# Optimization experiments

Measured on AMD Instinct MI355X. Metric: run time of the kernel, lower is better.

## Reference

```python
import jax, jax.numpy as jnp
import numpy as np

VOCAB, EMB = 32000, 300
B, T, S = 64, 25, 50
NF = 100
FS = (3, 4, 5)
H = 256
OUT = 31


def setup_inputs() -> dict:
    key = jax.random.key(0)
    ks = jax.random.split(key, 12)
    inp = {}
    inp["dialogue"] = jax.random.randint(ks[0], (B, T, S), 0, VOCAB)
    inp["emb"] = jax.random.normal(ks[1], (VOCAB, EMB), jnp.float32) * 0.1
    for j, fs in enumerate(FS):
        inp[f"conv_w{fs}"] = jax.random.normal(ks[2 + j], (NF, 1, fs, EMB), jnp.float32) * (1.0 / np.sqrt(fs * EMB))
        inp[f"conv_b{fs}"] = jnp.zeros((NF,), jnp.float32)
    IN = NF * len(FS)
    sc = 1.0 / np.sqrt(H)
    inp["wih"] = jax.random.normal(ks[5], (4 * H, IN), jnp.float32) * sc
    inp["whh"] = jax.random.normal(ks[6], (4 * H, H), jnp.float32) * sc
    inp["bih"] = jnp.zeros((4 * H,), jnp.float32)
    inp["bhh"] = jnp.zeros((4 * H,), jnp.float32)
    inp["wih_r"] = jax.random.normal(ks[7], (4 * H, IN), jnp.float32) * sc
    inp["whh_r"] = jax.random.normal(ks[8], (4 * H, H), jnp.float32) * sc
    inp["bih_r"] = jnp.zeros((4 * H,), jnp.float32)
    inp["bhh_r"] = jnp.zeros((4 * H,), jnp.float32)
    inp["h2o_w"] = jax.random.normal(ks[9], (OUT, 2 * H), jnp.float32) * sc
    inp["h2o_b"] = jnp.zeros((OUT,), jnp.float32)
    return inp


def _cnn_embed(tokens, emb, conv_params):
    # tokens: [B,T,S] int -> per-utterance CNN features [B,T, NF*len(FS)]
    x = emb[tokens.reshape(-1, S)]           # [B*T, S, EMB] embedding lookup
    x = x[:, None, :, :]                      # NCHW: [B*T, 1, S, EMB]
    feats = []
    for (w, b) in conv_params:
        c = jax.lax.conv_general_dilated(
            x, w, (1, 1), 'VALID', dimension_numbers=('NCHW', 'OIHW', 'NCHW'))
        c = jax.nn.relu(c + b[None, :, None, None])   # [B*T, NF, S-fs+1, 1]
        feats.append(jnp.max(c[..., 0], axis=2))      # max-pool over time -> [B*T, NF]
    return jnp.concatenate(feats, axis=1).reshape(B, T, -1)


def _lstm(x, wih, whh, bih, bhh):
    # single-layer LSTM, torch gate order (i, f, g, o); x: [B,Tm,I] -> [B,Tm,H]
    h0 = jnp.zeros((x.shape[0], H), x.dtype)

    def step(carry, xt):
        h, c = carry
        g = xt @ wih.T + h @ whh.T + bih + bhh        # [B, 4H]
        i, f, gg, o = jnp.split(g, 4, axis=-1)
        c = jax.nn.sigmoid(f) * c + jax.nn.sigmoid(i) * jnp.tanh(gg)
        h = jax.nn.sigmoid(o) * jnp.tanh(c)
        return (h, c), h

    _, hs = jax.lax.scan(step, (h0, h0), jnp.swapaxes(x, 0, 1))
    return jnp.swapaxes(hs, 0, 1)


def reference(dialogue, emb, conv_w3, conv_b3, conv_w4, conv_b4, conv_w5, conv_b5,
              wih, whh, bih, bhh, wih_r, whh_r, bih_r, bhh_r, h2o_w, h2o_b):
    r_in = _cnn_embed(dialogue, emb,
                      [(conv_w3, conv_b3), (conv_w4, conv_b4), (conv_w5, conv_b5)])
    # bi=True branch: self.rnn consumes the sequence in reverse order, outputs
    # stored back at their original positions == reverse, scan, reverse.
    rev = _lstm(r_in[:, ::-1], wih, whh, bih, bhh)[:, ::-1]
    # rnn_r consumes the sequence forward (teacher_forcing_ratio=None path)
    fwd = _lstm(r_in, wih_r, whh_r, bih_r, bhh_r)
    h = jnp.concatenate([rev, fwd], axis=-1)          # [B,T,2H]
    return jax.nn.sigmoid(h @ h2o_w.T + h2o_b)        # [B,T,OUT]
```

## Files before the change

### kernel.cpp

```cpp
#include <hip/hip_runtime.h>
#include <hip/hip_bf16.h>

#define NB 64
#define NT 25
#define NS 50
#define EMBD 300
#define NFILT 100
#define HD 256
#define NOUT 31
#define NBT (NB*NT)

#define KP3 928
#define KP4 1216
#define KP5 1504
#define XS_LEN 15104

typedef __attribute__((ext_vector_type(8))) short short8;
typedef __attribute__((ext_vector_type(4))) float f32x4;

__device__ __forceinline__ float hsum4(float4 a) { return (a.x + a.y) + (a.z + a.w); }
__device__ __forceinline__ void fma4(float4& a, float4 w, float4 x) {
    a.x = fmaf(w.x, x.x, a.x); a.y = fmaf(w.y, x.y, a.y);
    a.z = fmaf(w.z, x.z, a.z); a.w = fmaf(w.w, x.w, a.w);
}
__device__ __forceinline__ float sigmoidf_(float x) { return 1.0f / (1.0f + __expf(-x)); }
__device__ __forceinline__ float tanh_fast(float x) {
    x = fminf(fmaxf(x, -15.0f), 15.0f);
    const float e = __expf(2.0f * x);
    return (e - 1.0f) / (e + 1.0f);
}

__device__ __forceinline__ unsigned short f2bf(float f) {
    union { float f; unsigned u; } v; v.f = f;
    unsigned r = v.u + 0x7FFF + ((v.u >> 16) & 1);
    return (unsigned short)(r >> 16);
}

__device__ __forceinline__ short8 ld8_a8(const unsigned short* p) {
    short8 r;
    ((uint2*)&r)[0] = *(const uint2*)p;
    ((uint2*)&r)[1] = *(const uint2*)(p + 4);
    return r;
}

__global__ __launch_bounds__(256) void k_prep(
    const float* __restrict__ w3, const float* __restrict__ w4, const float* __restrict__ w5,
    unsigned short* __restrict__ wb)
{
    const int S0 = 112 * KP3, S1 = S0 + 112 * KP4, S2 = S1 + 112 * KP5;
    int idx = blockIdx.x * 256 + threadIdx.x;
    if (idx >= S2) return;
    int rel, Kp, K; const float* src;
    if (idx < S0)      { rel = idx;      Kp = KP3; K = 900;  src = w3; }
    else if (idx < S1) { rel = idx - S0; Kp = KP4; K = 1200; src = w4; }
    else               { rel = idx - S1; Kp = KP5; K = 1500; src = w5; }
    int f = rel / Kp, k = rel - f * Kp;
    float v = (f < NFILT && k < K) ? src[(size_t)f * K + k] : 0.0f;
    wb[idx] = f2bf(v);
}

__global__ __launch_bounds__(256) void k_prep2(
    const float* __restrict__ whh, const float* __restrict__ whh_r,
    unsigned short* __restrict__ wb2)
{
    const int idx = blockIdx.x * 256 + threadIdx.x;
    const int dir = idx >> 18;
    const int rem = idx & 262143;
    const int n = rem >> 8, k = rem & 255;
    const int j = n >> 2, gate = n & 3;
    const float* src = dir ? whh_r : whh;
    wb2[idx] = f2bf(src[(size_t)(gate * 256 + j) * 256 + k]);
}

__global__ __launch_bounds__(512) void k_conv(
    const int* __restrict__ tok, const float* __restrict__ emb,
    const unsigned short* __restrict__ wb,
    const float* __restrict__ b3, const float* __restrict__ b4, const float* __restrict__ b5,
    float* __restrict__ rin)
{
    __shared__ unsigned short xs[2][XS_LEN];
    const int bt0 = blockIdx.x * 2;
    const int tid = threadIdx.x;
    for (int i4 = tid; i4 < 2 * NS * 75; i4 += 512) {
        const int smp = i4 / (NS * 75);
        const int rem = i4 - smp * (NS * 75);
        const int s = rem / 75, e4 = rem - s * 75;
        const int t = tok[(bt0 + smp) * NS + s];
        float4 v = ((const float4*)(emb + (size_t)t * EMBD))[e4];
        uint2 pk;
        pk.x = (unsigned)f2bf(v.x) | ((unsigned)f2bf(v.y) << 16);
        pk.y = (unsigned)f2bf(v.z) | ((unsigned)f2bf(v.w) << 16);
        *(uint2*)(&xs[smp][s * 300 + e4 * 4]) = pk;
    }
    for (int i = NS * EMBD + tid; i < XS_LEN; i += 512) { xs[0][i] = 0; xs[1][i] = 0; }
    __syncthreads();

    const int wave = tid >> 6, lane = tid & 63;
    const int col = lane & 15, kg = lane >> 4;

    for (int job = wave; job < 21; job += 8) {
        const int fsi = job / 7, ntile = job - fsi * 7;
        int Kp, P, obase; const unsigned short* W; const float* bias;
        if (fsi == 0)      { Kp = KP3; P = 48; W = wb;                       bias = b3; obase = 0; }
        else if (fsi == 1) { Kp = KP4; P = 47; W = wb + 112 * KP3;           bias = b4; obase = NFILT; }
        else               { Kp = KP5; P = 46; W = wb + 112 * (KP3 + KP4);   bias = b5; obase = 2 * NFILT; }

        const unsigned short* wrow = W + (size_t)(ntile * 16 + col) * Kp + kg * 8;
        const unsigned short* xb0 = &xs[0][col * 300 + kg * 8];
        const unsigned short* xb1 = &xs[1][col * 300 + kg * 8];
        f32x4 a00 = {0,0,0,0}, a01 = {0,0,0,0}, a02 = {0,0,0,0};
        f32x4 a10 = {0,0,0,0}, a11 = {0,0,0,0}, a12 = {0,0,0,0};

        const int nks = Kp / 32;
        short8 wb0 = *(const short8*)(wrow);
        short8 wb1 = *(const short8*)(wrow + 32);
        for (int ks = 0; ks < nks; ++ks) {
            const int k0 = ks * 32;
            short8 bfrag = wb0;
            wb0 = wb1;
            if (ks + 2 < nks) wb1 = *(const short8*)(wrow + k0 + 64);
            short8 p0 = ld8_a8(xb0 + k0);
            short8 p1 = ld8_a8(xb0 + 16 * 300 + k0);
            short8 p2 = ld8_a8(xb0 + 32 * 300 + k0);
            short8 q0 = ld8_a8(xb1 + k0);
            short8 q1 = ld8_a8(xb1 + 16 * 300 + k0);
            short8 q2 = ld8_a8(xb1 + 32 * 300 + k0);
            a00 = __builtin_amdgcn_mfma_f32_16x16x32_bf16(p0, bfrag, a00, 0, 0, 0);
            a01 = __builtin_amdgcn_mfma_f32_16x16x32_bf16(p1, bfrag, a01, 0, 0, 0);
            a02 = __builtin_amdgcn_mfma_f32_16x16x32_bf16(p2, bfrag, a02, 0, 0, 0);
            a10 = __builtin_amdgcn_mfma_f32_16x16x32_bf16(q0, bfrag, a10, 0, 0, 0);
            a11 = __builtin_amdgcn_mfma_f32_16x16x32_bf16(q1, bfrag, a11, 0, 0, 0);
            a12 = __builtin_amdgcn_mfma_f32_16x16x32_bf16(q2, bfrag, a12, 0, 0, 0);
        }

        float pm0 = -1e30f, pm1 = -1e30f;
        #pragma unroll
        for (int reg = 0; reg < 4; ++reg) {
            pm0 = fmaxf(pm0, a00[reg]); pm0 = fmaxf(pm0, a01[reg]);
            pm1 = fmaxf(pm1, a10[reg]); pm1 = fmaxf(pm1, a11[reg]);
            const int r2 = 32 + kg * 4 + reg;
            if (r2 < P) { pm0 = fmaxf(pm0, a02[reg]); pm1 = fmaxf(pm1, a12[reg]); }
        }
        pm0 = fmaxf(pm0, __shfl_xor(pm0, 16, 64));
        pm0 = fmaxf(pm0, __shfl_xor(pm0, 32, 64));
        pm1 = fmaxf(pm1, __shfl_xor(pm1, 16, 64));
        pm1 = fmaxf(pm1, __shfl_xor(pm1, 32, 64));
        if (lane < 16) {
            const int f = ntile * 16 + lane;
            if (f < NFILT) {
                const float bb = bias[f];
                rin[(size_t)bt0 * (3 * NFILT) + obase + f]       = fmaxf(0.0f, pm0 + bb);
                rin[(size_t)(bt0 + 1) * (3 * NFILT) + obase + f] = fmaxf(0.0f, pm1 + bb);
            }
        }
    }
}

__global__ __launch_bounds__(256) void k_gin(
    const float* __restrict__ rin,
    const float* __restrict__ wih,   const float* __restrict__ bih,   const float* __restrict__ bhh,
    const float* __restrict__ wih_r, const float* __restrict__ bih_r, const float* __restrict__ bhh_r,
    float* __restrict__ gin)
{
    __shared__ float xsh[8 * EMBD];
    const int bt0 = blockIdx.x * 8;
    const int tid = threadIdx.x;
    const float4* src = (const float4*)(rin + (size_t)bt0 * EMBD);
    for (int i4 = tid; i4 < 8 * EMBD / 4; i4 += 256) ((float4*)xsh)[i4] = src[i4];
    __syncthreads();
    for (int g2 = tid; g2 < 2 * 1024; g2 += 256) {
        const int d = g2 >> 10;
        const int g = g2 & 1023;
        const float* wp = (d ? wih_r : wih) + (size_t)g * EMBD;
        const float bb = d ? (bih_r[g] + bhh_r[g]) : (bih[g] + bhh[g]);
        const float4* w4p = (const float4*)wp;
        float4 acc[8];
        #pragma unroll
        for (int r = 0; r < 8; ++r) acc[r] = {0,0,0,0};
        for (int k = 0; k < EMBD / 4; ++k) {
            const float4 wv = w4p[k];
            #pragma unroll
            for (int r = 0; r < 8; ++r) fma4(acc[r], wv, ((const float4*)(xsh + r * EMBD))[k]);
        }
        const int gp = ((g & 255) << 2) | (g >> 8);
        #pragma unroll
        for (int r = 0; r < 8; ++r) {
            const int bt = bt0 + r;
            const int b = bt / NT, t = bt - b * NT;
            gin[(((size_t)d * NT + t) * NB + b) * 1024 + gp] = hsum4(acc[r]) + bb;
        }
    }
}

__global__ __launch_bounds__(512, 2) void k_lstm(
    const float* __restrict__ gin,
    const unsigned short* __restrict__ wb2,
    float* __restrict__ hs)
{
    const int bid = blockIdx.x;
    const int dir = bid >> 2, bq = bid & 3;
    const int tid = threadIdx.x;
    const int wave = tid >> 6, lane = tid & 63;
    const int l15 = lane & 15, kg = lane >> 4;

    __shared__ unsigned short hb[2][16 * 264];
    __shared__ float slab[8][32 * 20];

    for (int i = tid; i < 16 * 264; i += 512) hb[0][i] = 0;
    __syncthreads();

    const unsigned short* wb_w = wb2 + (size_t)dir * (1024 * 256)
                               + (size_t)(wave * 128 + l15) * 256 + kg * 8;
    const float* gb = gin + (size_t)dir * (NT * NB * 1024);
    float* hsb = hs + (size_t)dir * NBT * HD;

    float c[8];
    #pragma unroll
    for (int q = 0; q < 8; ++q) c[q] = 0.0f;

    const int j_local = lane & 7;
    const int b_lo = (lane >> 3) & 7;

    for (int s = 0; s < NT; ++s) {
        const int t = dir ? s : (NT - 1 - s);
        const unsigned short* hc = hb[s & 1];
        unsigned short* hn = hb[(s + 1) & 1];

        float4 gxr[8];
        #pragma unroll
        for (int ntp = 0; ntp < 4; ++ntp)
            #pragma unroll
            for (int p = 0; p < 2; ++p) {
                const int b_row = b_lo + p * 8;
                const int bglob = bq * 16 + b_row;
                const int j_g = wave * 32 + ntp * 8 + j_local;
                gxr[ntp * 2 + p] = *(const float4*)(gb + (((size_t)t * NB + bglob) << 10) + j_g * 4);
            }

        short8 avb[8];
        #pragma unroll
        for (int kk = 0; kk < 8; ++kk)
            avb[kk] = *(const short8*)(hc + l15 * 264 + kk * 32 + kg * 8);

        f32x4 acc[8];
        #pragma unroll
        for (int nt = 0; nt < 8; ++nt) acc[nt] = (f32x4){0.f, 0.f, 0.f, 0.f};

        short8 wbuf[2][8];
        #pragma unroll
        for (int nt = 0; nt < 8; ++nt)
            wbuf[0][nt] = *(const short8*)(wb_w + nt * 4096);
        #pragma unroll
        for (int kk = 0; kk < 8; ++kk) {
            const int cur = kk & 1;
            if (kk < 7) {
                #pragma unroll
                for (int nt = 0; nt < 8; ++nt)
                    wbuf[cur ^ 1][nt] = *(const short8*)(wb_w + nt * 4096 + (kk + 1) * 32);
            }
            #pragma unroll
            for (int nt = 0; nt < 8; ++nt)
                acc[nt] = __builtin_amdgcn_mfma_f32_16x16x32_bf16(avb[kk], wbuf[cur][nt], acc[nt], 0, 0, 0);
        }

        float* sw = &slab[wave][0];
        #pragma unroll
        for (int ntp = 0; ntp < 4; ++ntp) {
            *(f32x4*)(sw + l15 * 20 + kg * 4)        = acc[2 * ntp];
            *(f32x4*)(sw + (16 + l15) * 20 + kg * 4) = acc[2 * ntp + 1];
            #pragma unroll
            for (int p = 0; p < 2; ++p) {
                const int b_row = b_lo + p * 8;
                const int bglob = bq * 16 + b_row;
                const int j_g = wave * 32 + ntp * 8 + j_local;
                const float gI = sw[(j_local * 4 + 0) * 20 + b_row];
                const float gF = sw[(j_local * 4 + 1) * 20 + b_row];
                const float gG = sw[(j_local * 4 + 2) * 20 + b_row];
                const float gO = sw[(j_local * 4 + 3) * 20 + b_row];
                const float4 gx = gxr[ntp * 2 + p];
                const float vi = sigmoidf_(gI + gx.x);
                const float vf = sigmoidf_(gF + gx.y);
                const float vg = tanh_fast(gG + gx.z);
                const float vo = sigmoidf_(gO + gx.w);
                const int ci = ntp * 2 + p;
                const float cc = vf * c[ci] + vi * vg;
                c[ci] = cc;
                const float hh = vo * tanh_fast(cc);
                hn[b_row * 264 + j_g] = f2bf(hh);
                hsb[((size_t)bglob * NT + t) * HD + j_g] = hh;
            }
        }
        __syncthreads();
    }
}

__global__ __launch_bounds__(64) void k_out(
    const float* __restrict__ hs, const float* __restrict__ w, const float* __restrict__ bias,
    float* __restrict__ out)
{
    __shared__ float hsh[2 * HD];
    const int bt = blockIdx.x;
    const int tid = threadIdx.x;
    const float4* rev4 = (const float4*)(hs + (size_t)bt * HD);
    const float4* fwd4 = (const float4*)(hs + ((size_t)NBT + bt) * HD);
    for (int i = tid; i < 2 * HD / 4; i += 64)
        ((float4*)hsh)[i] = (i < HD / 4) ? rev4[i] : fwd4[i - HD / 4];
    __syncthreads();
    if (tid < NOUT) {
        const float4* wr = (const float4*)(w + (size_t)tid * (2 * HD));
        float4 acc{0,0,0,0};
        for (int k = 0; k < 2 * HD / 4; ++k) fma4(acc, wr[k], ((const float4*)hsh)[k]);
        out[(size_t)bt * NOUT + tid] = sigmoidf_(hsum4(acc) + bias[tid]);
    }
}

extern "C" void kernel_launch(void* const* d_in, const int* in_sizes, int n_in,
                              void* d_out, int out_size, void* d_ws, size_t ws_size,
                              hipStream_t stream)
{
    const int*   tok   = (const int*)d_in[0];
    const float* emb   = (const float*)d_in[1];
    const float* w3    = (const float*)d_in[2];
    const float* b3    = (const float*)d_in[3];
    const float* w4    = (const float*)d_in[4];
    const float* b4    = (const float*)d_in[5];
    const float* w5    = (const float*)d_in[6];
    const float* b5    = (const float*)d_in[7];
    const float* wih   = (const float*)d_in[8];
    const float* whh   = (const float*)d_in[9];
    const float* bih   = (const float*)d_in[10];
    const float* bhh   = (const float*)d_in[11];
    const float* wih_r = (const float*)d_in[12];
    const float* whh_r = (const float*)d_in[13];
    const float* bih_r = (const float*)d_in[14];
    const float* bhh_r = (const float*)d_in[15];
    const float* h2o_w = (const float*)d_in[16];
    const float* h2o_b = (const float*)d_in[17];

    float* ws  = (float*)d_ws;
    float* rin = ws;
    float* gin = rin + (size_t)NBT * 3 * NFILT;
    float* hs  = gin + (size_t)2 * NBT * 1024;
    unsigned short* wb  = (unsigned short*)gin;
    unsigned short* wb2 = (unsigned short*)rin;

    k_prep <<<1596, 256, 0, stream>>>(w3, w4, w5, wb);
    k_conv <<<NBT / 2, 512, 0, stream>>>(tok, emb, wb, b3, b4, b5, rin);
    k_gin  <<<NBT / 8, 256, 0, stream>>>(rin, wih, bih, bhh, wih_r, bih_r, bhh_r, gin);
    k_prep2<<<2048, 256, 0, stream>>>(whh, whh_r, wb2);
    k_lstm <<<8, 512, 0, stream>>>(gin, wb2, hs);
    k_out  <<<NBT, 64, 0, stream>>>(hs, h2o_w, h2o_b, (float*)d_out);
}
```

Before: 510.2 us.

## Double LSTM block to 1024 threads, halving per-wave gate columns

The recurrent LSTM kernel now runs 16 waves per block instead of 8. Each wave handles 64 gate rows (16 hidden units) instead of 128, which halves the per-wave MFMA chain and the register footprint of each serial timestep. The weight prefetch is also restructured into a two-deep pipeline with loads issued after the MFMAs. This adds more waves contending at the per-step barrier and a larger LDS slab, while only 8 blocks still run.

Measured after the change: 514.0 us. Within noise of the previous version (+0.8%).

```diff
diff --git a/kernel.cpp b/kernel.cpp
--- a/kernel.cpp
+++ b/kernel.cpp
@@ -112,13 +112,13 @@
         f32x4 a10 = {0,0,0,0}, a11 = {0,0,0,0}, a12 = {0,0,0,0};
 
         const int nks = Kp / 32;
-        short8 wb0 = *(const short8*)(wrow);
-        short8 wb1 = *(const short8*)(wrow + 32);
+        short8 wr0 = *(const short8*)(wrow);
+        short8 wr1 = *(const short8*)(wrow + 32);
         for (int ks = 0; ks < nks; ++ks) {
             const int k0 = ks * 32;
-            short8 bfrag = wb0;
-            wb0 = wb1;
-            if (ks + 2 < nks) wb1 = *(const short8*)(wrow + k0 + 64);
+            short8 bfrag = wr0;
+            wr0 = wr1;
+            if (ks + 2 < nks) wr1 = *(const short8*)(wrow + k0 + 64);
             short8 p0 = ld8_a8(xb0 + k0);
             short8 p1 = ld8_a8(xb0 + 16 * 300 + k0);
             short8 p2 = ld8_a8(xb0 + 32 * 300 + k0);
@@ -192,7 +192,7 @@
     }
 }
 
-__global__ __launch_bounds__(512, 2) void k_lstm(
+__global__ __launch_bounds__(1024, 1) void k_lstm(
     const float* __restrict__ gin,
     const unsigned short* __restrict__ wb2,
     float* __restrict__ hs)
@@ -204,37 +204,35 @@
     const int l15 = lane & 15, kg = lane >> 4;
 
     __shared__ unsigned short hb[2][16 * 264];
-    __shared__ float slab[8][32 * 20];
-
-    for (int i = tid; i < 16 * 264; i += 512) hb[0][i] = 0;
+    __shared__ float slab[16][32 * 20];
+
+    for (int i = tid; i < 16 * 264; i += 1024) hb[0][i] = 0;
     __syncthreads();
 
     const unsigned short* wb_w = wb2 + (size_t)dir * (1024 * 256)
-                               + (size_t)(wave * 128 + l15) * 256 + kg * 8;
+                               + (size_t)(wave * 64 + l15) * 256 + kg * 8;
     const float* gb = gin + (size_t)dir * (NT * NB * 1024);
     float* hsb = hs + (size_t)dir * NBT * HD;
 
-    float c[8];
-    #pragma unroll
-    for (int q = 0; q < 8; ++q) c[q] = 0.0f;
+    float c[4] = {0.f, 0.f, 0.f, 0.f};
 
     const int j_local = lane & 7;
-    const int b_lo = (lane >> 3) & 7;
+    const int b_lo = lane >> 3;
 
     for (int s = 0; s < NT; ++s) {
         const int t = dir ? s : (NT - 1 - s);
         const unsigned short* hc = hb[s & 1];
         unsigned short* hn = hb[(s + 1) & 1];
 
-        float4 gxr[8];
-        #pragma unroll
-        for (int ntp = 0; ntp < 4; ++ntp)
+        float4 gxr[4];
+        #pragma unroll
+        for (int t2 = 0; t2 < 2; ++t2)
             #pragma unroll
             for (int p = 0; p < 2; ++p) {
                 const int b_row = b_lo + p * 8;
                 const int bglob = bq * 16 + b_row;
-                const int j_g = wave * 32 + ntp * 8 + j_local;
-                gxr[ntp * 2 + p] = *(const float4*)(gb + (((size_t)t * NB + bglob) << 10) + j_g * 4);
+                const int j_g = wave * 16 + t2 * 8 + j_local;
+                gxr[t2 * 2 + p] = *(const float4*)(gb + (((size_t)t * NB + bglob) << 10) + j_g * 4);
             }
 
         short8 avb[8];
@@ -242,47 +240,49 @@
         for (int kk = 0; kk < 8; ++kk)
             avb[kk] = *(const short8*)(hc + l15 * 264 + kk * 32 + kg * 8);
 
-        f32x4 acc[8];
-        #pragma unroll
-        for (int nt = 0; nt < 8; ++nt) acc[nt] = (f32x4){0.f, 0.f, 0.f, 0.f};
-
-        short8 wbuf[2][8];
-        #pragma unroll
-        for (int nt = 0; nt < 8; ++nt)
+        f32x4 acc[4];
+        #pragma unroll
+        for (int nt = 0; nt < 4; ++nt) acc[nt] = (f32x4){0.f, 0.f, 0.f, 0.f};
+
+        short8 wbuf[2][4];
+        #pragma unroll
+        for (int nt = 0; nt < 4; ++nt) {
             wbuf[0][nt] = *(const short8*)(wb_w + nt * 4096);
+            wbuf[1][nt] = *(const short8*)(wb_w + nt * 4096 + 32);
+        }
         #pragma unroll
         for (int kk = 0; kk < 8; ++kk) {
             const int cur = kk & 1;
-            if (kk < 7) {
+            #pragma unroll
+            for (int nt = 0; nt < 4; ++nt)
+                acc[nt] = __builtin_amdgcn_mfma_f32_16x16x32_bf16(avb[kk], wbuf[cur][nt], acc[nt], 0, 0, 0);
+            if (kk + 2 < 8) {
                 #pragma unroll
-                for (int nt = 0; nt < 8; ++nt)
-                    wbuf[cur ^ 1][nt] = *(const short8*)(wb_w + nt * 4096 + (kk + 1) * 32);
+                for (int nt = 0; nt < 4; ++nt)
+                    wbuf[cur][nt] = *(const short8*)(wb_w + nt * 4096 + (kk + 2) * 32);
             }
-            #pragma unroll
-            for (int nt = 0; nt < 8; ++nt)
-                acc[nt] = __builtin_amdgcn_mfma_f32_16x16x32_bf16(avb[kk], wbuf[cur][nt], acc[nt], 0, 0, 0);
         }
 
         float* sw = &slab[wave][0];
         #pragma unroll
-        for (int ntp = 0; ntp < 4; ++ntp) {
-            *(f32x4*)(sw + l15 * 20 + kg * 4)        = acc[2 * ntp];
-            *(f32x4*)(sw + (16 + l15) * 20 + kg * 4) = acc[2 * ntp + 1];
+        for (int t2 = 0; t2 < 2; ++t2) {
+            *(f32x4*)(sw + l15 * 20 + kg * 4)        = acc[2 * t2];
+            *(f32x4*)(sw + (16 + l15) * 20 + kg * 4) = acc[2 * t2 + 1];
             #pragma unroll
             for (int p = 0; p < 2; ++p) {
                 const int b_row = b_lo + p * 8;
                 const int bglob = bq * 16 + b_row;
-                const int j_g = wave * 32 + ntp * 8 + j_local;
+                const int j_g = wave * 16 + t2 * 8 + j_local;
                 const float gI = sw[(j_local * 4 + 0) * 20 + b_row];
                 const float gF = sw[(j_local * 4 + 1) * 20 + b_row];
                 const float gG = sw[(j_local * 4 + 2) * 20 + b_row];
                 const float gO = sw[(j_local * 4 + 3) * 20 + b_row];
-                const float4 gx = gxr[ntp * 2 + p];
+                const float4 gx = gxr[t2 * 2 + p];
                 const float vi = sigmoidf_(gI + gx.x);
                 const float vf = sigmoidf_(gF + gx.y);
                 const float vg = tanh_fast(gG + gx.z);
                 const float vo = sigmoidf_(gO + gx.w);
-                const int ci = ntp * 2 + p;
+                const int ci = t2 * 2 + p;
                 const float cc = vf * c[ci] + vi * vg;
                 c[ci] = cc;
                 const float hh = vo * tanh_fast(cc);
@@ -348,6 +348,6 @@
     k_conv <<<NBT / 2, 512, 0, stream>>>(tok, emb, wb, b3, b4, b5, rin);
     k_gin  <<<NBT / 8, 256, 0, stream>>>(rin, wih, bih, bhh, wih_r, bih_r, bhh_r, gin);
     k_prep2<<<2048, 256, 0, stream>>>(whh, whh_r, wb2);
-    k_lstm <<<8, 512, 0, stream>>>(gin, wb2, hs);
+    k_lstm <<<8, 1024, 0, stream>>>(gin, wb2, hs);
     k_out  <<<NBT, 64, 0, stream>>>(hs, h2o_w, h2o_b, (float*)d_out);
 }
```
